# Optimization experiments

Measured on AMD Instinct MI355X. Metric: run time of the kernel, lower is better.

Reference implementation:

```python
import jax, jax.numpy as jnp
import numpy as np

M_CENTER = 3.0  # diagonal value of the 'centers' matrix
OUT_HW = (513, 513)  # original input spatial size (input_shape in torch forward)


def _conv(x, w, dilation=1, padding=0):
    return jax.lax.conv_general_dilated(
        x, w, window_strides=(1, 1),
        padding=[(padding, padding), (padding, padding)],
        rhs_dilation=(dilation, dilation),
        dimension_numbers=("NCHW", "OIHW", "NCHW"))


def _resize(x, hw):
    return jax.image.resize(x, (x.shape[0], x.shape[1], hw[0], hw[1]), method="bilinear")


def _head(low_level, out, pw, w0, w1, w2, w3, pool_w, aproj_w, cw1, cw2, cb2):
    # DeepLabHeadV3Plus (BN folded to identity at inference: gamma=1, beta=0, mean=0, var=1)
    ll = jax.nn.relu(_conv(low_level, pw))                      # [N,48,129,129]
    branches = [jax.nn.relu(_conv(out, w0))]                    # 1x1 branch
    for w, d in zip((w1, w2, w3), (6, 12, 18)):
        branches.append(jax.nn.relu(_conv(out, w, dilation=d, padding=d)))
    gp = jnp.mean(out, axis=(2, 3), keepdims=True)              # AdaptiveAvgPool2d(1)
    gp = jax.nn.relu(_conv(gp, pool_w))
    gp = jnp.broadcast_to(gp, branches[0].shape)                # bilinear upsample of 1x1 == broadcast
    branches.append(gp)
    y = jax.nn.relu(_conv(jnp.concatenate(branches, axis=1), aproj_w))  # [N,256,33,33]
    y = _resize(y, (ll.shape[2], ll.shape[3]))                  # -> 129x129
    y = jnp.concatenate([ll, y], axis=1)                        # [N,304,129,129]
    y = jax.nn.relu(_conv(y, cw1, padding=1))
    y = _conv(y, cw2) + cb2[None, :, None, None]                # [N,C,129,129]
    return y


def _forward_single(x):
    # x: [N,C,129,129] head logits. Upsample, then squared-distance to diagonal centers (m*I).
    x = _resize(x, OUT_HW)                                      # [N,C,513,513]
    C = x.shape[1]
    features_out = jnp.transpose(x, (0, 2, 3, 1))               # NHWC, as in torch
    # dist2mean[...,c] = -sum_j (f_j - m*1[j==c])^2 = -(|f|^2 - 2*m*f_c + m^2)
    sumsq = jnp.sum(x * x, axis=1, keepdims=True)
    logits = 2.0 * M_CENTER * x - sumsq - M_CENTER * M_CENTER   # [N,C,513,513]
    centers = M_CENTER * jnp.eye(C, dtype=x.dtype)
    return logits, centers, features_out


def _kaiming(key, shape):
    fan_in = shape[1] * shape[2] * shape[3]
    return jax.random.normal(key, shape, jnp.float32) * np.sqrt(2.0 / fan_in)


def _head_params(key, num_classes):
    ks = jax.random.split(key, 10)
    return dict(
        pw=_kaiming(ks[0], (48, 256, 1, 1)),
        w0=_kaiming(ks[1], (256, 2048, 1, 1)),
        w1=_kaiming(ks[2], (256, 2048, 3, 3)),
        w2=_kaiming(ks[3], (256, 2048, 3, 3)),
        w3=_kaiming(ks[4], (256, 2048, 3, 3)),
        pool_w=_kaiming(ks[5], (256, 2048, 1, 1)),
        aproj_w=_kaiming(ks[6], (256, 1280, 1, 1)),
        cw1=_kaiming(ks[7], (256, 304, 3, 3)),
        cw2=_kaiming(ks[8], (num_classes, 256, 1, 1)),
        cb2=jnp.zeros((num_classes,), jnp.float32),
    )


def setup_inputs() -> dict:
    key = jax.random.key(0)
    k_ll, k_out, k_h0, k_h1 = jax.random.split(key, 4)
    inp = {
        "low_level": jax.random.normal(k_ll, (2, 256, 129, 129), jnp.float32),
        "out": jax.random.normal(k_out, (2, 2048, 33, 33), jnp.float32),
    }
    for pref, k, nc in (("h0_", k_h0, 16), ("h1_", k_h1, 17)):
        for name, v in _head_params(k, nc).items():
            inp[pref + name] = v
    return inp


def reference(low_level, out,
              h0_pw, h0_w0, h0_w1, h0_w2, h0_w3, h0_pool_w, h0_aproj_w, h0_cw1, h0_cw2, h0_cb2,
              h1_pw, h1_w0, h1_w1, h1_w2, h1_w3, h1_pool_w, h1_aproj_w, h1_cw1, h1_cw2, h1_cb2):
    x0 = _head(low_level, out, h0_pw, h0_w0, h0_w1, h0_w2, h0_w3, h0_pool_w, h0_aproj_w, h0_cw1, h0_cw2, h0_cb2)
    x1 = _head(low_level, out, h1_pw, h1_w0, h1_w1, h1_w2, h1_w3, h1_pool_w, h1_aproj_w, h1_cw1, h1_cw2, h1_cb2)
    l0, c0, f0 = _forward_single(x0)
    l1, c1, f1 = _forward_single(x1)
    return (l0, l1, c0, c1, f0, f1)
```

## Files before the change

### kernel.cpp

```cpp
#include <hip/hip_runtime.h>

#define TPB 256

typedef _Float16 f16;
typedef __attribute__((ext_vector_type(8))) _Float16 f16x8;
typedef __attribute__((ext_vector_type(16))) float f32x16;

#define GLD_LDS(g, l) __builtin_amdgcn_global_load_lds( \
    (const __attribute__((address_space(1))) void*)(g), \
    (__attribute__((address_space(3))) void*)(l), 16, 0, 0)

__global__ __launch_bounds__(TPB)
void tcz_k(const float* __restrict__ aspp, const float* __restrict__ ll,
           f16* __restrict__ Xa, f16* __restrict__ Xll)
{
    const int bid = blockIdx.x;
    const int tid = threadIdx.x;
    const float* src; f16* dst; int C, HW, ldk, pT, cT, bb;
    if (bid < 4480) {
        src = aspp; dst = Xa; C = 2048; HW = 1089; ldk = 2048;
        pT = bid % 35; cT = (bid / 35) % 64; bb = bid / 2240;
    } else {
        const int b2 = bid - 4480;
        src = ll; dst = Xll; C = 256; HW = 16641; ldk = 256;
        pT = b2 % 521; cT = (b2 / 521) % 8; bb = b2 / 4168;
    }
    __shared__ float t32[32 * 33];
#pragma unroll
    for (int pass = 0; pass < 4; ++pass) {
        const int ch = tid / 32 + pass * 8;
        const int px = tid % 32;
        const int c = cT * 32 + ch, p = pT * 32 + px;
        float v = 0.f;
        if (c < C && p < HW) v = src[((long)bb * C + c) * HW + p];
        t32[ch * 33 + px] = v;
    }
    __syncthreads();
#pragma unroll
    for (int pass = 0; pass < 4; ++pass) {
        const int px = tid / 32 + pass * 8;
        const int ch = tid % 32;
        const int p = pT * 32 + px, c = cT * 32 + ch;
        if (p < HW && c < C)
            dst[((long)bb * HW + p) * ldk + c] = (f16)t32[ch * 33 + px];
    }
}

__global__ __launch_bounds__(TPB)
void tcr_k(const f16* __restrict__ part, f16* __restrict__ dst)
{
    __shared__ float t32[32 * 33];
    const int pT = blockIdx.x, cT = blockIdx.y, bb = blockIdx.z;
    const int tid = threadIdx.x;
    const int br = cT >> 3;
    const f16* pb = part + (long)bb * 2787840;
#pragma unroll
    for (int pass = 0; pass < 4; ++pass) {
        const int ch = tid / 32 + pass * 8;
        const int px = tid % 32;
        const int c = cT * 32 + ch;
        const int cl = c & 255;
        const int p = pT * 32 + px;
        float v = 0.f;
        if (p < 1089) {
            if (br == 0) {
                v = (float)pb[(long)cl * 1089 + p];
            } else {
                const int dl = 6 * br;
                const int y = p / 33;
                const int s0 = 1 + 3 * (br - 1);
#pragma unroll
                for (int g = 0; g < 3; ++g) {
                    const int dy0 = (g - 1) * dl;
                    const int yLo = max(0, -dy0), yHi = min(33, 33 - dy0);
                    if (y >= yLo && y < yHi)
                        v += (float)pb[((long)(s0 + g) * 256 + cl) * 1089 + p];
                }
            }
            v = fmaxf(v, 0.f);
        }
        t32[ch * 33 + px] = v;
    }
    __syncthreads();
#pragma unroll
    for (int pass = 0; pass < 4; ++pass) {
        const int px = tid / 32 + pass * 8;
        const int ch = tid % 32;
        const int p = pT * 32 + px, c = cT * 32 + ch;
        if (p < 1089)
            dst[((long)bb * 1089 + p) * 1024 + c] = (f16)t32[ch * 33 + px];
    }
}

__global__ __launch_bounds__(TPB)
void gpool_k(const float* __restrict__ in, float* __restrict__ gp, int HW, float inv)
{
    const int bc = blockIdx.x;
    const float* p = in + (size_t)bc * HW;
    float s = 0.f;
    for (int i = threadIdx.x; i < HW; i += TPB) s += p[i];
#pragma unroll
    for (int off = 32; off > 0; off >>= 1) s += __shfl_down(s, off, 64);
    __shared__ float red[4];
    if ((threadIdx.x & 63) == 0) red[threadIdx.x >> 6] = s;
    __syncthreads();
    if (threadIdx.x == 0) gp[bc] = (red[0] + red[1] + red[2] + red[3]) * inv;
}

__global__ __launch_bounds__(TPB)
void gemv1_k(const float* __restrict__ pw0, const float* __restrict__ pw1,
             const float* __restrict__ gp, float* __restrict__ gpr2)
{
    const int bh = blockIdx.x & 3;
    const int cgrp = blockIdx.x >> 2;
    const int b = bh & 1;
    const float* w = (bh >> 1) ? pw1 : pw0;
    const int c = cgrp * 16 + (threadIdx.x >> 4);
    const int kl = threadIdx.x & 15;
    const float* g = gp + (size_t)b * 2048;
    float4 acc = {0.f, 0.f, 0.f, 0.f};
    for (int k = kl * 4; k < 2048; k += 64) {
        const float4 wv = *(const float4*)&w[(size_t)c * 2048 + k];
        const float4 gv = *(const float4*)&g[k];
        acc.x = fmaf(wv.x, gv.x, acc.x);
        acc.y = fmaf(wv.y, gv.y, acc.y);
        acc.z = fmaf(wv.z, gv.z, acc.z);
        acc.w = fmaf(wv.w, gv.w, acc.w);
    }
    float s = (acc.x + acc.y) + (acc.z + acc.w);
#pragma unroll
    for (int o = 8; o; o >>= 1) s += __shfl_xor(s, o, 16);
    if (kl == 0) gpr2[bh * 256 + c] = fmaxf(s, 0.f);
}

__global__ __launch_bounds__(TPB)
void gemv2_k(const float* __restrict__ ap0, const float* __restrict__ ap1,
             const float* __restrict__ gpr2, float* __restrict__ gpc2)
{
    const int bh = blockIdx.x & 3;
    const int cgrp = blockIdx.x >> 2;
    const float* w = (bh >> 1) ? ap1 : ap0;
    const int c = cgrp * 16 + (threadIdx.x >> 4);
    const int kl = threadIdx.x & 15;
    const float* g = gpr2 + bh * 256;
    float4 acc = {0.f, 0.f, 0.f, 0.f};
    for (int k = kl * 4; k < 256; k += 64) {
        const float4 wv = *(const float4*)&w[(size_t)c * 1280 + 1024 + k];
        const float4 gv = *(const float4*)&g[k];
        acc.x = fmaf(wv.x, gv.x, acc.x);
        acc.y = fmaf(wv.y, gv.y, acc.y);
        acc.z = fmaf(wv.z, gv.z, acc.z);
        acc.w = fmaf(wv.w, gv.w, acc.w);
    }
    float s = (acc.x + acc.y) + (acc.z + acc.w);
#pragma unroll
    for (int o = 8; o; o >>= 1) s += __shfl_xor(s, o, 16);
    if (kl == 0) gpc2[bh * 256 + c] = s;
}

struct PackJob { const float* w; f16* dst; int Cout, CinUse, CinSrc, T, coP, KB, start; };
struct PackParams { PackJob j[14]; };

__global__ __launch_bounds__(TPB)
void packw_mega(PackParams P, float* __restrict__ guard)
{
    const int bid = blockIdx.x;
    const int tid = threadIdx.x;
    if (bid >= 4832) {
        float4 zv = {0.f, 0.f, 0.f, 0.f};
        float4* p = (float4*)(guard + tid * 16);
        p[0] = zv; p[1] = zv; p[2] = zv; p[3] = zv;
        return;
    }
    int ji = 0;
#pragma unroll
    for (int t = 1; t < 14; ++t) if (bid >= P.j[t].start) ji = t;
    PackJob J;
    switch (ji) {
        case 0:  J = P.j[0];  break;
        case 1:  J = P.j[1];  break;
        case 2:  J = P.j[2];  break;
        case 3:  J = P.j[3];  break;
        case 4:  J = P.j[4];  break;
        case 5:  J = P.j[5];  break;
        case 6:  J = P.j[6];  break;
        case 7:  J = P.j[7];  break;
        case 8:  J = P.j[8];  break;
        case 9:  J = P.j[9];  break;
        case 10: J = P.j[10]; break;
        case 11: J = P.j[11]; break;
        case 12: J = P.j[12]; break;
        default: J = P.j[13]; break;
    }
    const int local = bid - J.start;
    const int kb = local % J.KB;
    const int coT = local / J.KB;
    const int T = J.T;
    __shared__ float tile[16 * 577];
    const int RL = 64 * T;
    const int n = 16 * RL;
    for (int idx = tid; idx < n; idx += TPB) {
        const int row = idx / RL;
        const int jj = idx - row * RL;
        const int co = coT * 16 + row;
        const int k = kb * 64 + jj / T;
        float v = 0.f;
        if (co < J.Cout && k < J.CinUse)
            v = J.w[((long)co * J.CinSrc + kb * 64) * T + jj];
        tile[row * 577 + jj] = v;
    }
    __syncthreads();
    const int nst = 128 * T;
    for (int idx = tid; idx < nst; idx += TPB) {
        const int g = idx & 7;
        const int t = (idx >> 3) % T;
        const int co = idx / (8 * T);
        f16x8 hv;
#pragma unroll
        for (int e = 0; e < 8; ++e)
            hv[e] = (f16)tile[co * 577 + (g * 8 + e) * T + t];
        *(f16x8*)&J.dst[(((long)t * J.KB + kb) * J.coP + coT * 16 + co) * 64 + g * 8] = hv;
    }
}

template <int OUTMODE, int ZMAP, int RELUOUT, int BIAS>
__global__ __launch_bounds__(TPB, 4)
void mconv(const f16* __restrict__ X, const f16* __restrict__ Wp,
           const f16* __restrict__ guard, void* __restrict__ out_,
           const float* __restrict__ gpc,
           int Cinp, int Cout, int H, int W, int kss_, int dl_,
           int kbPerTap, int tapCnt_,
           long xHstr, long wHstr, long oHstr, long outBStride,
           int coP, int ldOut, int NT, int NM, int NBH, int NZ)
{
    __shared__ char SH[32768];
    const int tid = threadIdx.x;

    int wg;
    {
        const int orig = blockIdx.x, nwg = gridDim.x;
        const int q = nwg >> 3, r = nwg & 7;
        const int xcd = orig & 7, off = orig >> 3;
        wg = (xcd < r ? xcd * (q + 1) : r * (q + 1) + (xcd - r) * q) + off;
    }
    const int nt = wg % NT; wg /= NT;
    const int mt = wg % NM; wg /= NM;
    const int bh = wg % NBH; wg /= NBH;
    const int z  = wg;
    const int b = bh & 1, hd = bh >> 1;
    const int co0 = mt * 128;
    const int NP = H * W;
    const long xBstr = (long)NP * Cinp;

    int kss = kss_, dl = dl_, tapStart = 0, tapCnt = tapCnt_;
    long woff = (long)hd * wHstr, ooff = (long)hd * oHstr;
    int p0 = nt * 128, pMax = NP;
    if (ZMAP == 1) {
        int br, grp;
        if (z == 0) { br = 0; grp = 1; kss = 1; dl = 1; tapStart = 0; tapCnt = 1; }
        else { br = 1 + (z - 1) / 3; grp = (z - 1) % 3;
               kss = 3; dl = (br == 1) ? 6 : (br == 2 ? 12 : 18);
               tapStart = grp * 3; tapCnt = 3; }
        woff += (br == 0) ? 0L : (br == 1 ? 524288L : (br == 2 ? 5242880L : 9961472L));
        ooff += (long)z * 278784L;
        const int dy0 = (kss == 1) ? 0 : (grp - 1) * dl;
        const int yLo = max(0, -dy0), yHi = min(H, H - dy0);
        p0 = yLo * W + nt * 128;
        pMax = yHi * W;
        if (p0 >= pMax) return;
    }
    const int half = kss >> 1;
    const int y0t = p0 / W, y1t = min(p0 + 127, pMax - 1) / W;

    int taps[9]; int nval = 0;
    for (int t = 0; t < tapCnt; ++t) {
        const int tp = tapStart + t;
        const int ky = tp / kss;
        const int dy = (ky - half) * dl;
        if (ZMAP == 1 || (y1t + dy >= 0 && y0t + dy < H)) taps[nval++] = tp;
    }
    if (nval == 0) return;

    const int srow = tid >> 3;
    const int sslot = tid & 7;
    int aofs[4];
#pragma unroll
    for (int q = 0; q < 4; ++q) {
        const int row = q * 32 + srow;
        aofs[q] = row * 64 + ((sslot ^ (row & 7)) << 3);
    }
    const long coStr = (long)coP * 64;

    const int lane = tid & 63, wid = tid >> 6;
    const int wm = wid >> 1, wn = wid & 1;
    const int r32 = lane & 31, hh = lane >> 5;
    const int arow0 = wm * 64 + r32, arow1 = arow0 + 32;
    const int brow0 = wn * 64 + r32, brow1 = brow0 + 32;
    const int abase0 = arow0 * 128, abase1 = arow1 * 128;
    const int bbase0 = 16384 + brow0 * 128, bbase1 = 16384 + brow1 * 128;
    const int ax0 = (arow0 & 7), ax1 = (arow1 & 7);
    const int bx0 = (brow0 & 7), bx1 = (brow1 & 7);

    f32x16 acc[2][2];
#pragma unroll
    for (int i = 0; i < 2; ++i)
#pragma unroll
        for (int j = 0; j < 2; ++j) acc[i][j] = (f32x16)(0.f);

    const f16* Pr[4];
    for (int ti = 0; ti < nval; ++ti) {
        const int tp = taps[ti];
        const int ky = tp / kss, kx = tp - ky * kss;
        const int dy = (ky - half) * dl, dx = (kx - half) * dl;
#pragma unroll
        for (int q = 0; q < 4; ++q) {
            const int row = q * 32 + srow;
            const int p = p0 + row;
            bool v = p < pMax;
            const int py = v ? p / W : 0;
            const int px = v ? p - py * W : 0;
            const int sy = py + dy, sx = px + dx;
            v = v && ((unsigned)sy < (unsigned)H) && ((unsigned)sx < (unsigned)W);
            const int swz = (sslot ^ (row & 7)) << 3;
            Pr[q] = v ? (X + (long)b * xBstr + (long)hd * xHstr
                           + ((long)sy * W + sx) * (long)Cinp + swz)
                      : (guard + swz);
        }
        const f16* Wt = Wp + woff + ((long)tp * kbPerTap * coP + (long)co0) * 64;
        for (int kb = 0; kb < kbPerTap; ++kb) {
            __syncthreads();
            const f16* wsrc = Wt + (long)kb * coStr;
            const long kcol = (long)kb << 6;
            GLD_LDS(wsrc + aofs[0], SH + (tid << 4));
            GLD_LDS(wsrc + aofs[1], SH + 4096 + (tid << 4));
            GLD_LDS(wsrc + aofs[2], SH + 8192 + (tid << 4));
            GLD_LDS(wsrc + aofs[3], SH + 12288 + (tid << 4));
            GLD_LDS(Pr[0] + kcol, SH + 16384 + (tid << 4));
            GLD_LDS(Pr[1] + kcol, SH + 20480 + (tid << 4));
            GLD_LDS(Pr[2] + kcol, SH + 24576 + (tid << 4));
            GLD_LDS(Pr[3] + kcol, SH + 28672 + (tid << 4));
            __syncthreads();
            __builtin_amdgcn_s_setprio(1);
#pragma unroll
            for (int kh = 0; kh < 4; ++kh) {
                const int g = kh * 2 + hh;
                const f16x8 a0 = *(const f16x8*)(SH + abase0 + ((g ^ ax0) << 4));
                const f16x8 a1 = *(const f16x8*)(SH + abase1 + ((g ^ ax1) << 4));
                const f16x8 b0 = *(const f16x8*)(SH + bbase0 + ((g ^ bx0) << 4));
                const f16x8 b1 = *(const f16x8*)(SH + bbase1 + ((g ^ bx1) << 4));
                acc[0][0] = __builtin_amdgcn_mfma_f32_32x32x16_f16(a0, b0, acc[0][0], 0, 0, 0);
                acc[0][1] = __builtin_amdgcn_mfma_f32_32x32x16_f16(a0, b1, acc[0][1], 0, 0, 0);
                acc[1][0] = __builtin_amdgcn_mfma_f32_32x32x16_f16(a1, b0, acc[1][0], 0, 0, 0);
                acc[1][1] = __builtin_amdgcn_mfma_f32_32x32x16_f16(a1, b1, acc[1][1], 0, 0, 0);
            }
            __builtin_amdgcn_s_setprio(0);
        }
    }

    const long outB = (long)b * outBStride + ooff;
    const float* gpcp = BIAS ? (gpc + (long)(b + 2 * hd) * 256) : nullptr;
#pragma unroll
    for (int mi = 0; mi < 2; ++mi)
#pragma unroll
    for (int ni = 0; ni < 2; ++ni)
#pragma unroll
    for (int j = 0; j < 16; ++j) {
        const int m = wm * 64 + mi * 32 + 4 * hh + (j & 3) + 8 * (j >> 2);
        const int n = wn * 64 + ni * 32 + r32;
        const int co = co0 + m;
        const int p = p0 + n;
        if (co < Cout && p < pMax) {
            float v = acc[mi][ni][j];
            if (BIAS) v += gpcp[co];
            if (RELUOUT) v = fmaxf(v, 0.f);
            if (OUTMODE == 1) ((f16*)out_)[outB + (long)co * NP + p] = (f16)v;
            else              ((f16*)out_)[outB + (long)p * ldOut + co] = (f16)v;
        }
    }
}

__global__ __launch_bounds__(TPB)
void ups2pad_k(const f16* __restrict__ ybx, f16* __restrict__ ccx)
{
    const int idx = blockIdx.x * TPB + threadIdx.x;
    if (idx >= 4 * 16641 * 34) return;
    const int s = idx / (16641 * 34);
    const int rem = idx - s * (16641 * 34);
    const int p = rem / 34;
    const int cg = rem - p * 34;
    if (cg >= 32) {
        f16x8 zv = (f16x8)(f16)0.f;
        *(f16x8*)(ccx + ((long)s * 16641 + p) * 320 + 304 + (cg - 32) * 8) = zv;
        return;
    }
    const int oy = p / 129, ox = p % 129;
    const float sc = 33.0f / 129.0f;
    const float sx = (ox + 0.5f) * sc - 0.5f;
    const float sy = (oy + 0.5f) * sc - 0.5f;
    int ix0 = (int)floorf(sx), iy0 = (int)floorf(sy);
    const float fx = sx - ix0, fy = sy - iy0;
    int ix1 = min(32, max(0, ix0 + 1)); ix0 = min(32, max(0, ix0));
    int iy1 = min(32, max(0, iy0 + 1)); iy0 = min(32, max(0, iy0));
    const f16* base = ybx + (long)s * 1089 * 256 + cg * 8;
    const f16x8 v00 = *(const f16x8*)(base + ((long)iy0 * 33 + ix0) * 256);
    const f16x8 v01 = *(const f16x8*)(base + ((long)iy0 * 33 + ix1) * 256);
    const f16x8 v10 = *(const f16x8*)(base + ((long)iy1 * 33 + ix0) * 256);
    const f16x8 v11 = *(const f16x8*)(base + ((long)iy1 * 33 + ix1) * 256);
    f16x8 r;
#pragma unroll
    for (int e = 0; e < 8; ++e) {
        const float a0 = (float)v00[e] + ((float)v01[e] - (float)v00[e]) * fx;
        const float a1 = (float)v10[e] + ((float)v11[e] - (float)v10[e]) * fx;
        r[e] = (f16)(a0 + (a1 - a0) * fy);
    }
    *(f16x8*)(ccx + ((long)s * 16641 + p) * 320 + 48 + cg * 8) = r;
}

__global__ __launch_bounds__(TPB)
void conv1x1_m(const f16* __restrict__ c1o2,
               const float* __restrict__ w0, const float* __restrict__ w1,
               const float* __restrict__ b0, const float* __restrict__ b1,
               float* __restrict__ xb2)
{
    const int h = blockIdx.z;
    const int nc = h ? 17 : 16;
    const float* w = h ? w1 : w0;
    const float* bias = h ? b1 : b0;
    __shared__ float wsm[256 * 17];
    __shared__ float bsm[17];
    const int tid = threadIdx.x;
    for (int l = tid; l < 256 * 17; l += TPB) {
        const int k = l / 17, c = l - k * 17;
        wsm[l] = (c < nc) ? w[(size_t)c * 256 + k] : 0.f;
    }
    if (tid < nc) bsm[tid] = bias[tid];
    __syncthreads();
    const int b = blockIdx.y;
    const int p = blockIdx.x * TPB + tid;
    if (p >= 16641) return;
    const f16* inB = c1o2 + (long)h * 8520192 + (long)b * 4260096 + p;
    float acc[17];
#pragma unroll
    for (int c = 0; c < 17; ++c) acc[c] = 0.f;
    for (int k = 0; k < 256; ++k) {
        const float x = (float)inB[(size_t)k * 16641];
#pragma unroll
        for (int c = 0; c < 17; ++c) acc[c] = fmaf(wsm[k * 17 + c], x, acc[c]);
    }
    float* oB = xb2 + (h ? 532512L : 0L) + ((long)b * nc) * 16641 + p;
#pragma unroll
    for (int c = 0; c < 17; ++c)
        if (c < nc) oB[(size_t)c * 16641] = acc[c] + bsm[c];
}

__global__ __launch_bounds__(TPB)
void final_m(const float* __restrict__ xb2, float* __restrict__ o)
{
    const int idx = blockIdx.x * TPB + threadIdx.x;
    if (idx >= 2 * 526338) return;
    const int hd = idx / 526338;
    int r = idx - hd * 526338;
    const int ox = r % 513; r /= 513;
    const int oy = r % 513;
    const int b = r / 513;
    const int nc = hd ? 17 : 16;
    const long HW = 513L * 513L;
    const float sc = 129.0f / 513.0f;
    const float sx = (ox + 0.5f) * sc - 0.5f;
    const float sy = (oy + 0.5f) * sc - 0.5f;
    int ix0 = (int)floorf(sx), iy0 = (int)floorf(sy);
    const float fx = sx - ix0, fy = sy - iy0;
    int ix1 = min(128, max(0, ix0 + 1)); ix0 = min(128, max(0, ix0));
    int iy1 = min(128, max(0, iy0 + 1)); iy0 = min(128, max(0, iy0));
    const float* xb = xb2 + (hd ? 532512L : 0L) + (size_t)b * nc * 16641;
    const int i00 = iy0 * 129 + ix0, i01 = iy0 * 129 + ix1;
    const int i10 = iy1 * 129 + ix0, i11 = iy1 * 129 + ix1;
    float* logits = o + (hd ? 8421408L : 0L);
    float* feats  = o + (hd ? 25791107L : 17369699L);
    float v[17];
    float ss = 0.f;
#pragma unroll
    for (int c = 0; c < 17; ++c) {
        if (c < nc) {
            const float* s = xb + (size_t)c * 16641;
            const float a0 = s[i00] + (s[i01] - s[i00]) * fx;
            const float a1 = s[i10] + (s[i11] - s[i10]) * fx;
            const float vv = a0 + (a1 - a0) * fy;
            v[c] = vv;
            ss = fmaf(vv, vv, ss);
        }
    }
    const long pix = (long)oy * 513 + ox;
#pragma unroll
    for (int c = 0; c < 17; ++c)
        if (c < nc)
            logits[((size_t)b * nc + c) * HW + pix] = fmaf(6.f, v[c], -ss - 9.f);
    float* f = feats + ((size_t)b * HW + pix) * nc;
#pragma unroll
    for (int c = 0; c < 17; ++c)
        if (c < nc) f[c] = v[c];
}

__global__ void centers_k(float* __restrict__ c0, float* __restrict__ c1)
{
    const int t = blockIdx.x * 64 + threadIdx.x;
    if (t < 256) c0[t] = (t / 16 == t % 16) ? 3.f : 0.f;
    const int u = t - 256;
    if (u >= 0 && u < 289) c1[u] = (u / 17 == u % 17) ? 3.f : 0.f;
}

extern "C" void kernel_launch(void* const* d_in, const int* in_sizes, int n_in,
                              void* d_out, int out_size, void* d_ws, size_t ws_size,
                              hipStream_t stream)
{
    const float* low_level = (const float*)d_in[0];
    const float* aspp_in   = (const float*)d_in[1];
    float* ws = (float*)d_ws;
    float* o  = (float*)d_out;

    float* GUARDF  = ws + 0;
    f16*   GUARD   = (f16*)GUARDF;
    f16*   Apack2  = (f16*)(ws + 4096);
    f16*   C1O2    = (f16*)(ws + 4096);
    f16*   AprojP2 = (f16*)(ws + 14684160);
    f16*   Cw1P2   = (f16*)(ws + 14946304);
    f16*   LlP2    = (f16*)(ws + 15683584);
    f16*   Xa      = (f16*)(ws + 15716352);
    f16*   BRpart  = (f16*)(ws + 17946624);
    f16*   BRX2    = (f16*)(ws + 23522304);
    f16*   YBX2    = (f16*)(ws + 25752576);
    float* XB2     = ws + 26310144;
    float* GP      = ws + 27408450;
    float* GPC2    = ws + 27412546;
    float* GPR2    = ws + 27413570;

    f16*   CCX2    = (f16*)(o + 0);
    f16*   Xll     = (f16*)(o + 10650240);

    const long C0o = 17369154, C1oo = 17369410;

    tcz_k<<<12816, TPB, 0, stream>>>(aspp_in, low_level, Xa, Xll);
    gpool_k<<<4096, TPB, 0, stream>>>(aspp_in, GP, 1089, 1.0f / 1089.0f);
    gemv1_k<<<64, TPB, 0, stream>>>(
        (const float*)d_in[2 + 5], (const float*)d_in[2 + 10 + 5], GP, GPR2);
    gemv2_k<<<64, TPB, 0, stream>>>(
        (const float*)d_in[2 + 6], (const float*)d_in[2 + 10 + 6], GPR2, GPC2);

    PackParams P;
    int start = 0;
    for (int h = 0; h < 2; ++h) {
        const float* pw    = (const float*)d_in[2 + h * 10 + 0];
        const float* w0    = (const float*)d_in[2 + h * 10 + 1];
        const float* w1    = (const float*)d_in[2 + h * 10 + 2];
        const float* w2    = (const float*)d_in[2 + h * 10 + 3];
        const float* w3    = (const float*)d_in[2 + h * 10 + 4];
        const float* aproj = (const float*)d_in[2 + h * 10 + 6];
        const float* cw1   = (const float*)d_in[2 + h * 10 + 7];
        f16* Ap = Apack2 + (long)h * 14680064;
        const PackJob jobs[7] = {
            { w0,    Ap,                          256, 2048, 2048, 1, 256, 32, 0 },
            { w1,    Ap + 524288,                 256, 2048, 2048, 9, 256, 32, 0 },
            { w2,    Ap + 5242880,                256, 2048, 2048, 9, 256, 32, 0 },
            { w3,    Ap + 9961472,                256, 2048, 2048, 9, 256, 32, 0 },
            { aproj, AprojP2 + (long)h * 262144,  256, 1024, 1280, 1, 256, 16, 0 },
            { cw1,   Cw1P2 + (long)h * 737280,    256,  304,  304, 9, 256,  5, 0 },
            { pw,    LlP2 + (long)h * 32768,       48,  256,  256, 1, 128,  4, 0 },
        };
        for (int t = 0; t < 7; ++t) {
            P.j[h * 7 + t] = jobs[t];
            P.j[h * 7 + t].start = start;
            start += jobs[t].KB * (jobs[t].coP / 16);
        }
    }
    packw_mega<<<4833, TPB, 0, stream>>>(P, GUARDF);

    mconv<1, 1, 0, 0><<<720, TPB, 0, stream>>>(
        Xa, Apack2, GUARD, BRpart, nullptr, 2048, 256, 33, 33, 3, 1,
        32, 0, 0L, 14680064L, 5575680L, 2787840L, 256, 0, 9, 2, 4, 10);
    tcr_k<<<dim3(35, 32, 4), TPB, 0, stream>>>(BRpart, BRX2);
    mconv<3, 0, 1, 1><<<72, TPB, 0, stream>>>(
        BRX2, AprojP2, GUARD, YBX2, GPC2, 1024, 256, 33, 33, 1, 1,
        16, 1, 2230272L, 262144L, 557568L, 278784L, 256, 256, 9, 2, 4, 1);
    mconv<3, 0, 1, 0><<<524, TPB, 0, stream>>>(
        Xll, LlP2, GUARD, CCX2, nullptr, 256, 48, 129, 129, 1, 1,
        4, 1, 0L, 32768L, 10650240L, 5325120L, 128, 320, 131, 1, 4, 1);
    ups2pad_k<<<8841, TPB, 0, stream>>>(YBX2, CCX2);
    mconv<1, 0, 1, 0><<<1048, TPB, 0, stream>>>(
        CCX2, Cw1P2, GUARD, C1O2, nullptr, 320, 256, 129, 129, 3, 1,
        5, 9, 10650240L, 737280L, 8520192L, 4260096L, 256, 0, 131, 2, 4, 1);
    conv1x1_m<<<dim3(66, 2, 2), TPB, 0, stream>>>(C1O2,
        (const float*)d_in[2 + 8], (const float*)d_in[2 + 10 + 8],
        (const float*)d_in[2 + 9], (const float*)d_in[2 + 10 + 9], XB2);
    final_m<<<4113, TPB, 0, stream>>>(XB2, o);
    centers_k<<<9, 64, 0, stream>>>(o + C0o, o + C1oo);
}
```

Baseline: 635.2 us.

## Split ASPP conv K-dimension across two workgroups and fold global pooling into transpose kernel

The ASPP dilated-conv launch now splits each tap's K-blocks into two halves, doubling the grid and writing two partial outputs that the reduction kernel tcr_k sums. This is meant to raise parallelism and fill more CUs on the small 33x33 problem. It costs extra partial-buffer traffic, which is moved into the output scratch area. Separately, the global average pooling kernel is merged into the transpose kernel as extra blocks, saving one launch.

```diff
diff --git a/kernel.cpp b/kernel.cpp
--- a/kernel.cpp
+++ b/kernel.cpp
@@ -12,10 +12,24 @@
 
 __global__ __launch_bounds__(TPB)
 void tcz_k(const float* __restrict__ aspp, const float* __restrict__ ll,
-           f16* __restrict__ Xa, f16* __restrict__ Xll)
+           f16* __restrict__ Xa, f16* __restrict__ Xll, float* __restrict__ gp)
 {
     const int bid = blockIdx.x;
     const int tid = threadIdx.x;
+    __shared__ float t32[32 * 33];
+    __shared__ float red[4];
+    if (bid >= 12816) {
+        const int bc = bid - 12816;
+        const float* p = aspp + (size_t)bc * 1089;
+        float s = 0.f;
+        for (int i = tid; i < 1089; i += TPB) s += p[i];
+#pragma unroll
+        for (int off = 32; off > 0; off >>= 1) s += __shfl_down(s, off, 64);
+        if ((tid & 63) == 0) red[tid >> 6] = s;
+        __syncthreads();
+        if (tid == 0) gp[bc] = (red[0] + red[1] + red[2] + red[3]) * (1.0f / 1089.0f);
+        return;
+    }
     const float* src; f16* dst; int C, HW, ldk, pT, cT, bb;
     if (bid < 4480) {
         src = aspp; dst = Xa; C = 2048; HW = 1089; ldk = 2048;
@@ -25,7 +39,6 @@
         src = ll; dst = Xll; C = 256; HW = 16641; ldk = 256;
         pT = b2 % 521; cT = (b2 / 521) % 8; bb = b2 / 4168;
     }
-    __shared__ float t32[32 * 33];
 #pragma unroll
     for (int pass = 0; pass < 4; ++pass) {
         const int ch = tid / 32 + pass * 8;
@@ -53,7 +66,7 @@
     const int pT = blockIdx.x, cT = blockIdx.y, bb = blockIdx.z;
     const int tid = threadIdx.x;
     const int br = cT >> 3;
-    const f16* pb = part + (long)bb * 2787840;
+    const f16* pb = part + (long)bb * 5575680;
 #pragma unroll
     for (int pass = 0; pass < 4; ++pass) {
         const int ch = tid / 32 + pass * 8;
@@ -63,18 +76,20 @@
         const int p = pT * 32 + px;
         float v = 0.f;
         if (p < 1089) {
+            const long cp = (long)cl * 1089 + p;
             if (br == 0) {
-                v = (float)pb[(long)cl * 1089 + p];
+                v = (float)pb[cp] + (float)pb[278784 + cp];
             } else {
                 const int dl = 6 * br;
                 const int y = p / 33;
-                const int s0 = 1 + 3 * (br - 1);
 #pragma unroll
                 for (int g = 0; g < 3; ++g) {
                     const int dy0 = (g - 1) * dl;
                     const int yLo = max(0, -dy0), yHi = min(33, 33 - dy0);
-                    if (y >= yLo && y < yHi)
-                        v += (float)pb[((long)(s0 + g) * 256 + cl) * 1089 + p];
+                    if (y >= yLo && y < yHi) {
+                        const long s0 = (long)(2 * (1 + 3 * (br - 1) + g)) * 278784;
+                        v += (float)pb[s0 + cp] + (float)pb[s0 + 278784 + cp];
+                    }
                 }
             }
             v = fmaxf(v, 0.f);
@@ -90,21 +105,6 @@
         if (p < 1089)
             dst[((long)bb * 1089 + p) * 1024 + c] = (f16)t32[ch * 33 + px];
     }
-}
-
-__global__ __launch_bounds__(TPB)
-void gpool_k(const float* __restrict__ in, float* __restrict__ gp, int HW, float inv)
-{
-    const int bc = blockIdx.x;
-    const float* p = in + (size_t)bc * HW;
-    float s = 0.f;
-    for (int i = threadIdx.x; i < HW; i += TPB) s += p[i];
-#pragma unroll
-    for (int off = 32; off > 0; off >>= 1) s += __shfl_down(s, off, 64);
-    __shared__ float red[4];
-    if ((threadIdx.x & 63) == 0) red[threadIdx.x >> 6] = s;
-    __syncthreads();
-    if (threadIdx.x == 0) gp[bc] = (red[0] + red[1] + red[2] + red[3]) * inv;
 }
 
 __global__ __launch_bounds__(TPB)
@@ -253,16 +253,20 @@
     const long xBstr = (long)NP * Cinp;
 
     int kss = kss_, dl = dl_, tapStart = 0, tapCnt = tapCnt_;
+    int kbB = 0, kbE = kbPerTap;
     long woff = (long)hd * wHstr, ooff = (long)hd * oHstr;
     int p0 = nt * 128, pMax = NP;
     if (ZMAP == 1) {
+        const int zg = z >> 1, khf = z & 1;
         int br, grp;
-        if (z == 0) { br = 0; grp = 1; kss = 1; dl = 1; tapStart = 0; tapCnt = 1; }
-        else { br = 1 + (z - 1) / 3; grp = (z - 1) % 3;
+        if (zg == 0) { br = 0; grp = 1; kss = 1; dl = 1; tapStart = 0; tapCnt = 1; }
+        else { br = 1 + (zg - 1) / 3; grp = (zg - 1) % 3;
                kss = 3; dl = (br == 1) ? 6 : (br == 2 ? 12 : 18);
                tapStart = grp * 3; tapCnt = 3; }
         woff += (br == 0) ? 0L : (br == 1 ? 524288L : (br == 2 ? 5242880L : 9961472L));
         ooff += (long)z * 278784L;
+        kbB = khf * (kbPerTap >> 1);
+        kbE = kbB + (kbPerTap >> 1);
         const int dy0 = (kss == 1) ? 0 : (grp - 1) * dl;
         const int yLo = max(0, -dy0), yHi = min(H, H - dy0);
         p0 = yLo * W + nt * 128;
@@ -327,7 +331,7 @@
                       : (guard + swz);
         }
         const f16* Wt = Wp + woff + ((long)tp * kbPerTap * coP + (long)co0) * 64;
-        for (int kb = 0; kb < kbPerTap; ++kb) {
+        for (int kb = kbB; kb < kbE; ++kb) {
             __syncthreads();
             const f16* wsrc = Wt + (long)kb * coStr;
             const long kcol = (long)kb << 6;
@@ -526,21 +530,20 @@
     f16*   Cw1P2   = (f16*)(ws + 14946304);
     f16*   LlP2    = (f16*)(ws + 15683584);
     f16*   Xa      = (f16*)(ws + 15716352);
-    f16*   BRpart  = (f16*)(ws + 17946624);
-    f16*   BRX2    = (f16*)(ws + 23522304);
-    f16*   YBX2    = (f16*)(ws + 25752576);
-    float* XB2     = ws + 26310144;
-    float* GP      = ws + 27408450;
-    float* GPC2    = ws + 27412546;
-    float* GPR2    = ws + 27413570;
+    f16*   BRX2    = (f16*)(ws + 17946624);
+    f16*   YBX2    = (f16*)(ws + 20176896);
+    float* XB2     = ws + 20734464;
+    float* GP      = ws + 21832770;
+    float* GPC2    = ws + 21836866;
+    float* GPR2    = ws + 21837890;
 
     f16*   CCX2    = (f16*)(o + 0);
     f16*   Xll     = (f16*)(o + 10650240);
+    f16*   BRpart  = (f16*)(o + 14910336);
 
     const long C0o = 17369154, C1oo = 17369410;
 
-    tcz_k<<<12816, TPB, 0, stream>>>(aspp_in, low_level, Xa, Xll);
-    gpool_k<<<4096, TPB, 0, stream>>>(aspp_in, GP, 1089, 1.0f / 1089.0f);
+    tcz_k<<<16912, TPB, 0, stream>>>(aspp_in, low_level, Xa, Xll, GP);
     gemv1_k<<<64, TPB, 0, stream>>>(
         (const float*)d_in[2 + 5], (const float*)d_in[2 + 10 + 5], GP, GPR2);
     gemv2_k<<<64, TPB, 0, stream>>>(
@@ -574,9 +577,9 @@
     }
     packw_mega<<<4833, TPB, 0, stream>>>(P, GUARDF);
 
-    mconv<1, 1, 0, 0><<<720, TPB, 0, stream>>>(
+    mconv<1, 1, 0, 0><<<1440, TPB, 0, stream>>>(
         Xa, Apack2, GUARD, BRpart, nullptr, 2048, 256, 33, 33, 3, 1,
-        32, 0, 0L, 14680064L, 5575680L, 2787840L, 256, 0, 9, 2, 4, 10);
+        32, 0, 0L, 14680064L, 11151360L, 5575680L, 256, 0, 9, 2, 4, 20);
     tcr_k<<<dim3(35, 32, 4), TPB, 0, stream>>>(BRpart, BRX2);
     mconv<3, 0, 1, 1><<<72, TPB, 0, stream>>>(
         BRX2, AprojP2, GUARD, YBX2, GPC2, 1024, 256, 33, 33, 1, 1,
```

Result: no change. 633.8 us (-0.2%).
